# Kernel tuning notes

Hardware: AMD Instinct MI355X
Metric: run time of the kernel (lower is better)

Reference implementation:

```python
import jax, jax.numpy as jnp
import numpy as np
import math

B_CAPS, C_CAPS, K, P, STRIDE, ITERS = 32, 32, 3, 4, 2, 3
PSIZE = P * P
EPS = 1e-8
LAMBDA = 1e-3
LN_2PI = math.log(2.0 * math.pi)


def setup_inputs() -> dict:
    key = jax.random.key(0)
    k1, k2 = jax.random.split(key)
    # input: (b, h, w, B*(P*P+1)); activations must be non-negative (sigmoid-range)
    x = jax.random.uniform(k1, (4, 16, 16, B_CAPS * (PSIZE + 1)), dtype=jnp.float32)
    # nn.Parameter(torch.randn(1, K*K*B, P, P))
    weights = jax.random.normal(k2, (1, K * K * B_CAPS, P, P), dtype=jnp.float32)
    beta_u = jnp.zeros((C_CAPS,), jnp.float32)
    beta_a = jnp.zeros((C_CAPS,), jnp.float32)
    return {"x": x, "weights": weights, "beta_u": beta_u, "beta_a": beta_a}


def _add_patches(x):
    # torch add_pathes: zero-pad 1 on each side, gather KxK patches with stride
    b, h, w, c = x.shape
    x = jnp.pad(x, ((0, 0), (1, 1), (1, 1), (0, 0)))
    hp = h + 2
    oh = (hp - K) // STRIDE + 1
    idxs = np.arange(0, hp - K + 1, STRIDE)[:, None] + np.arange(K)[None, :]  # (oh, K)
    x = x[:, idxs, :, :]        # (b, oh, K, hp, c)
    x = x[:, :, :, idxs, :]     # (b, oh, K, ow, K, c)
    x = jnp.transpose(x, (0, 1, 3, 2, 4, 5))  # (b, oh, ow, K, K, c)
    return x, oh, oh


def _m_step(a_in, r, v, beta_u, beta_a):
    # a_in: (n, Bk, 1), r: (n, Bk, C), v: (n, Bk, C, psize)
    n = v.shape[0]
    r = r * a_in
    r = r / (jnp.sum(r, axis=2, keepdims=True) + EPS)
    r_sum = jnp.sum(r, axis=1, keepdims=True)              # (n, 1, C)
    coeff = (r / (r_sum + EPS))[..., None]                 # (n, Bk, C, 1)
    mu = jnp.sum(coeff * v, axis=1, keepdims=True)         # (n, 1, C, psize)
    sigma_sq = jnp.sum(coeff * (v - mu) ** 2, axis=1, keepdims=True) + EPS
    # cost_h: (n, C, psize)
    cost_h = (beta_u[:, None] + jnp.log(jnp.sqrt(sigma_sq[:, 0]))) * jnp.transpose(r_sum, (0, 2, 1))
    a_out = jax.nn.sigmoid(LAMBDA * (beta_a - jnp.sum(cost_h, axis=2)))  # (n, C)
    return a_out, mu, sigma_sq


def _e_step(mu, sigma_sq, a_out, v):
    ln_p = -(v - mu) ** 2 / (2.0 * sigma_sq) - jnp.log(jnp.sqrt(sigma_sq)) - 0.5 * LN_2PI
    ln_ap = jnp.sum(ln_p, axis=3) + jnp.log(a_out)[:, None, :]  # (n, Bk, C)
    return jax.nn.softmax(ln_ap, axis=2)


def _em_routing(v, a_in, beta_u, beta_a):
    n, Bk, C, _ = v.shape
    r = jnp.full((n, Bk, C), 1.0 / C, dtype=v.dtype)
    mu = a_out = None
    for it in range(ITERS):
        a_out, mu, sigma_sq = _m_step(a_in, r, v, beta_u, beta_a)
        if it < ITERS - 1:
            r = _e_step(mu, sigma_sq, a_out, v)
    return mu, a_out


def reference(x, weights, beta_u, beta_a):
    b = x.shape[0]
    patches, oh, ow = _add_patches(x)                       # (b, oh, ow, K, K, B*(psize+1))
    n = b * oh * ow
    Bk = K * K * B_CAPS
    p_in = patches[..., : B_CAPS * PSIZE].reshape(n, Bk, P, P)
    a_in = patches[..., B_CAPS * PSIZE :].reshape(n, Bk, 1)
    # votes: pose_i @ W_i (weights have no C axis in this repo -> shared across out-caps)
    v = jnp.einsum("nipq,iqr->nipr", p_in, weights[0]).reshape(n, Bk, 1, PSIZE)
    v = jnp.broadcast_to(v, (n, Bk, C_CAPS, PSIZE))
    mu, a_out = _em_routing(v, a_in, beta_u, beta_a)
    p_out = mu.reshape(b, oh, ow, C_CAPS * PSIZE)
    a_out = a_out.reshape(b, oh, ow, C_CAPS)
    return jnp.concatenate([p_out, a_out], axis=-1)        # (b, oh, ow, C*(psize+1))
```

## Files before the change

### kernel.cpp

```cpp
#include <hip/hip_runtime.h>
#include <math.h>

#define NTH 1024

__launch_bounds__(NTH, 4)
__global__ void convcaps_em_kernel(const float* __restrict__ x,
                                   const float* __restrict__ wts,
                                   const float* __restrict__ beta_u,
                                   const float* __restrict__ beta_a,
                                   float* __restrict__ out) {
  constexpr int BK = 288;
  constexpr float EPS = 1e-8f;
  constexpr float LAM = 1e-3f;

  __shared__ __align__(16) float v_lds[BK * 16];
  __shared__ float r_lds[BK * 32];
  __shared__ float w_lds[BK];
  __shared__ float part_lds[32 * 32];
  __shared__ float rsum_lds[32];
  __shared__ __align__(16) float cstat_lds[8 * 32 * 4 * 8];
  __shared__ __align__(8) float muinv_lds[16 * 32 * 2];
  __shared__ float lnac_lds[32];

  const int t = threadIdx.x;
  const int n = blockIdx.x;
  const int b  = n >> 6;
  const int oy = (n >> 3) & 7;
  const int ox = n & 7;

  if (t < BK) {
    const int kk = t >> 5, cap = t & 31;
    const int kh = kk / 3, kw = kk - kh * 3;
    const int iy = oy * 2 - 1 + kh, ix = ox * 2 - 1 + kw;
    float val = 0.0f;
    if ((unsigned)iy < 16u && (unsigned)ix < 16u)
      val = x[(((b * 16 + iy) * 16) + ix) * 544 + 512 + cap];
    w_lds[t] = val / (val + EPS);
  }
  for (int task = t; task < BK * 4; task += NTH) {
    const int i = task >> 2, p = task & 3;
    const int kk = i >> 5, cap = i & 31;
    const int kh = kk / 3, kw = kk - kh * 3;
    const int iy = oy * 2 - 1 + kh, ix = ox * 2 - 1 + kw;
    float4 vv = make_float4(0.f, 0.f, 0.f, 0.f);
    if ((unsigned)iy < 16u && (unsigned)ix < 16u) {
      const float* px = x + ((((b * 16 + iy) * 16) + ix) * 544 + cap * 16 + p * 4);
      const float4 pin = *reinterpret_cast<const float4*>(px);
      const float* pw = wts + i * 16;
      const float4 w0 = *reinterpret_cast<const float4*>(pw + 0);
      const float4 w1 = *reinterpret_cast<const float4*>(pw + 4);
      const float4 w2 = *reinterpret_cast<const float4*>(pw + 8);
      const float4 w3 = *reinterpret_cast<const float4*>(pw + 12);
      vv.x = pin.x * w0.x + pin.y * w1.x + pin.z * w2.x + pin.w * w3.x;
      vv.y = pin.x * w0.y + pin.y * w1.y + pin.z * w2.y + pin.w * w3.y;
      vv.z = pin.x * w0.z + pin.y * w1.z + pin.z * w2.z + pin.w * w3.z;
      vv.w = pin.x * w0.w + pin.y * w1.w + pin.z * w2.w + pin.w * w3.w;
    }
    *reinterpret_cast<float4*>(&v_lds[i * 16 + p * 4]) = vv;
  }
  __syncthreads();

  const int c32 = t & 31;
  const int g32 = t >> 5;

  {
    float colsum = 0.0f;
    #pragma unroll
    for (int pass = 0; pass < 9; ++pass) {
      const int i = pass * 32 + g32;
      const float rv = w_lds[i] * 0.03125f;
      r_lds[i * 32 + c32] = rv;
      colsum += rv;
    }
    part_lds[g32 * 32 + c32] = colsum;
  }
  __syncthreads();

  const int pq = (t >> 5) & 3;
  const int hC = t >> 7;
  const int cS = (t >> 4) & 31;
  const int pS = t & 15;
  const float bu = beta_u[cS];
  const float ba = beta_a[cS];

  for (int it = 0; it < 3; ++it) {
    if (t < 32) {
      float s = 0.0f;
      #pragma unroll
      for (int g = 0; g < 32; ++g) s += part_lds[g * 32 + t];
      rsum_lds[t] = s;
    }
    {
      float4 s1 = make_float4(0.f, 0.f, 0.f, 0.f);
      float4 s2 = make_float4(0.f, 0.f, 0.f, 0.f);
      const int ib = hC * 36;
      #pragma unroll 6
      for (int k = 0; k < 36; ++k) {
        const int i = ib + k;
        const float r = r_lds[i * 32 + c32];
        const float4 v4 = *reinterpret_cast<const float4*>(&v_lds[i * 16 + pq * 4]);
        s1.x = fmaf(r, v4.x, s1.x); s2.x = fmaf(r * v4.x, v4.x, s2.x);
        s1.y = fmaf(r, v4.y, s1.y); s2.y = fmaf(r * v4.y, v4.y, s2.y);
        s1.z = fmaf(r, v4.z, s1.z); s2.z = fmaf(r * v4.z, v4.z, s2.z);
        s1.w = fmaf(r, v4.w, s1.w); s2.w = fmaf(r * v4.w, v4.w, s2.w);
      }
      float* cs = &cstat_lds[(hC * 128 + c32 * 4 + pq) * 8];
      *reinterpret_cast<float4*>(cs + 0) = s1;
      *reinterpret_cast<float4*>(cs + 4) = s2;
    }
    __syncthreads();

    if (t < 512) {
      float s1 = 0.0f, s2 = 0.0f;
      #pragma unroll
      for (int h = 0; h < 8; ++h) {
        const float* cs = &cstat_lds[(h * 128 + cS * 4 + (pS >> 2)) * 8 + (pS & 3)];
        s1 += cs[0];
        s2 += cs[4];
      }
      const float rs = rsum_lds[cS];
      const float D  = rs + EPS;
      const float mu = s1 / D;
      float sig = (s2 - mu * (2.0f * s1 - mu * rs)) / D;
      sig = fmaxf(sig, 0.0f) + EPS;
      const float lhalf = 0.5f * logf(sig);
      float lsum = lhalf;
      #pragma unroll
      for (int m = 8; m >= 1; m >>= 1) lsum += __shfl_xor(lsum, m, 16);
      const float z = LAM * (ba - rs * (16.0f * bu + lsum));
      const float aout = 1.0f / (1.0f + expf(-z));
      if (it < 2) {
        *reinterpret_cast<float2*>(&muinv_lds[(pS * 32 + cS) * 2]) =
            make_float2(mu, 0.5f / sig);
        if (pS == 0) lnac_lds[cS] = logf(aout) - lsum;
      } else {
        out[n * 544 + t] = mu;
        if (pS == 0) out[n * 544 + 512 + cS] = aout;
      }
    }

    if (it < 2) {
      __syncthreads();
      float muc[16], isc[16];
      #pragma unroll
      for (int p2 = 0; p2 < 16; ++p2) {
        const float2 mi =
            *reinterpret_cast<const float2*>(&muinv_lds[(p2 * 32 + c32) * 2]);
        muc[p2] = mi.x;
        isc[p2] = mi.y;
      }
      const float lna = lnac_lds[c32];
      float colsum = 0.0f;
      #pragma unroll 3
      for (int pass = 0; pass < 9; ++pass) {
        const int i = pass * 32 + g32;
        const float4 v0 = *reinterpret_cast<const float4*>(&v_lds[i * 16 + 0]);
        const float4 v1 = *reinterpret_cast<const float4*>(&v_lds[i * 16 + 4]);
        const float4 v2 = *reinterpret_cast<const float4*>(&v_lds[i * 16 + 8]);
        const float4 v3 = *reinterpret_cast<const float4*>(&v_lds[i * 16 + 12]);
        float acc = 0.0f, d;
        d = v0.x - muc[0];  acc = fmaf(d * d, isc[0],  acc);
        d = v0.y - muc[1];  acc = fmaf(d * d, isc[1],  acc);
        d = v0.z - muc[2];  acc = fmaf(d * d, isc[2],  acc);
        d = v0.w - muc[3];  acc = fmaf(d * d, isc[3],  acc);
        d = v1.x - muc[4];  acc = fmaf(d * d, isc[4],  acc);
        d = v1.y - muc[5];  acc = fmaf(d * d, isc[5],  acc);
        d = v1.z - muc[6];  acc = fmaf(d * d, isc[6],  acc);
        d = v1.w - muc[7];  acc = fmaf(d * d, isc[7],  acc);
        d = v2.x - muc[8];  acc = fmaf(d * d, isc[8],  acc);
        d = v2.y - muc[9];  acc = fmaf(d * d, isc[9],  acc);
        d = v2.z - muc[10]; acc = fmaf(d * d, isc[10], acc);
        d = v2.w - muc[11]; acc = fmaf(d * d, isc[11], acc);
        d = v3.x - muc[12]; acc = fmaf(d * d, isc[12], acc);
        d = v3.y - muc[13]; acc = fmaf(d * d, isc[13], acc);
        d = v3.z - muc[14]; acc = fmaf(d * d, isc[14], acc);
        d = v3.w - muc[15]; acc = fmaf(d * d, isc[15], acc);
        const float lnap = lna - acc;
        float mx = lnap;
        #pragma unroll
        for (int m = 16; m >= 1; m >>= 1) mx = fmaxf(mx, __shfl_xor(mx, m, 32));
        const float e = expf(lnap - mx);
        float ss = e;
        #pragma unroll
        for (int m = 16; m >= 1; m >>= 1) ss += __shfl_xor(ss, m, 32);
        const float rn = e * (w_lds[i] / ss);
        r_lds[i * 32 + c32] = rn;
        colsum += rn;
      }
      part_lds[g32 * 32 + c32] = colsum;
      __syncthreads();
    }
  }
}

extern "C" void kernel_launch(void* const* d_in, const int* in_sizes, int n_in,
                              void* d_out, int out_size, void* d_ws, size_t ws_size,
                              hipStream_t stream) {
  const float* x   = (const float*)d_in[0];
  const float* wts = (const float*)d_in[1];
  const float* bu  = (const float*)d_in[2];
  const float* ba  = (const float*)d_in[3];
  float* out = (float*)d_out;
  hipLaunchKernelGGL(convcaps_em_kernel, dim3(256), dim3(NTH), 0, stream,
                     x, wts, bu, ba, out);
}
```

Before: 84.97 us.

## Fuse E-step with M-step accumulation and specialize uniform first M-step

The first M-step is specialized for uniform initial routing: statistics are computed once per pose element and broadcast to all output capsules, instead of running the full per-capsule reduction. Each later E-step now accumulates the weighted first and second moments directly in registers and adds them into shared memory with LDS atomics. This removes the r_lds buffer and the separate M-step pass over v_lds. Fast intrinsics (__expf, __logf) replace expf and logf, trading a little accuracy and adding register pressure and atomic contention.

```diff
diff --git a/kernel.cpp b/kernel.cpp
--- a/kernel.cpp
+++ b/kernel.cpp
@@ -14,13 +14,14 @@
   constexpr float LAM = 1e-3f;
 
   __shared__ __align__(16) float v_lds[BK * 16];
-  __shared__ float r_lds[BK * 32];
   __shared__ float w_lds[BK];
-  __shared__ float part_lds[32 * 32];
+  __shared__ __align__(8) float part_lds[32 * 32];
   __shared__ float rsum_lds[32];
-  __shared__ __align__(16) float cstat_lds[8 * 32 * 4 * 8];
+  __shared__ float s1a_lds[16 * 32];
+  __shared__ float s2a_lds[16 * 32];
   __shared__ __align__(8) float muinv_lds[16 * 32 * 2];
   __shared__ float lnac_lds[32];
+  __shared__ float mu0_lds[16], i2s0_lds[16], sc0_lds[2];
 
   const int t = threadIdx.x;
   const int n = blockIdx.x;
@@ -62,103 +63,82 @@
 
   const int c32 = t & 31;
   const int g32 = t >> 5;
-
-  {
-    float colsum = 0.0f;
-    #pragma unroll
-    for (int pass = 0; pass < 9; ++pass) {
-      const int i = pass * 32 + g32;
-      const float rv = w_lds[i] * 0.03125f;
-      r_lds[i * 32 + c32] = rv;
-      colsum += rv;
-    }
-    part_lds[g32 * 32 + c32] = colsum;
-  }
-  __syncthreads();
-
-  const int pq = (t >> 5) & 3;
-  const int hC = t >> 7;
-  const int cS = (t >> 4) & 31;
-  const int pS = t & 15;
+  const int cS  = (t >> 4) & 31;
+  const int pS  = t & 15;
   const float bu = beta_u[cS];
   const float ba = beta_a[cS];
 
-  for (int it = 0; it < 3; ++it) {
-    if (t < 32) {
-      float s = 0.0f;
-      #pragma unroll
-      for (int g = 0; g < 32; ++g) s += part_lds[g * 32 + t];
-      rsum_lds[t] = s;
-    }
+  if (t < 512) {
+    const int h = t >> 4;
+    float aw = 0.f, a1 = 0.f, a2 = 0.f;
+    #pragma unroll
+    for (int k = 0; k < 9; ++k) {
+      const int i = h * 9 + k;
+      const float wv = w_lds[i];
+      const float vv = v_lds[i * 16 + pS];
+      aw += wv;
+      a1 = fmaf(wv, vv, a1);
+      a2 = fmaf(wv * vv, vv, a2);
+    }
+    *reinterpret_cast<float2*>(&part_lds[(h * 16 + pS) * 2]) = make_float2(a1, a2);
+    if (pS == 0) rsum_lds[h] = aw;
+  }
+  __syncthreads();
+  if (t < 16) {
+    float m0 = 0.f, a1 = 0.f, a2 = 0.f;
+    #pragma unroll
+    for (int h = 0; h < 32; ++h) {
+      m0 += rsum_lds[h];
+      const float2 f2 = *reinterpret_cast<const float2*>(&part_lds[(h * 16 + t) * 2]);
+      a1 += f2.x; a2 += f2.y;
+    }
+    const float D0 = m0 + 32.f * EPS;
+    const float mu = a1 / D0;
+    float sig = (a2 - mu * (2.f * a1 - mu * m0)) / D0;
+    sig = fmaxf(sig, 0.f) + EPS;
+    float ls = 0.5f * __logf(sig);
+    #pragma unroll
+    for (int m = 8; m >= 1; m >>= 1) ls += __shfl_xor(ls, m, 16);
+    mu0_lds[t] = mu;
+    i2s0_lds[t] = 0.5f / sig;
+    if (t == 0) { sc0_lds[0] = m0 * 0.03125f; sc0_lds[1] = ls; }
+  }
+  __syncthreads();
+  if (t < 512) {
+    *reinterpret_cast<float2*>(&muinv_lds[(pS * 32 + cS) * 2]) =
+        make_float2(mu0_lds[pS], i2s0_lds[pS]);
+    s1a_lds[t] = 0.f;
+    s2a_lds[t] = 0.f;
+    if (pS == 0) {
+      const float rs0 = sc0_lds[0], ls = sc0_lds[1];
+      const float z = LAM * (ba - rs0 * (16.f * bu + ls));
+      lnac_lds[cS] = -__logf(1.f + __expf(-z)) - ls;
+    }
+  }
+  __syncthreads();
+
+  for (int it = 0; it < 2; ++it) {
     {
-      float4 s1 = make_float4(0.f, 0.f, 0.f, 0.f);
-      float4 s2 = make_float4(0.f, 0.f, 0.f, 0.f);
-      const int ib = hC * 36;
-      #pragma unroll 6
-      for (int k = 0; k < 36; ++k) {
-        const int i = ib + k;
-        const float r = r_lds[i * 32 + c32];
-        const float4 v4 = *reinterpret_cast<const float4*>(&v_lds[i * 16 + pq * 4]);
-        s1.x = fmaf(r, v4.x, s1.x); s2.x = fmaf(r * v4.x, v4.x, s2.x);
-        s1.y = fmaf(r, v4.y, s1.y); s2.y = fmaf(r * v4.y, v4.y, s2.y);
-        s1.z = fmaf(r, v4.z, s1.z); s2.z = fmaf(r * v4.z, v4.z, s2.z);
-        s1.w = fmaf(r, v4.w, s1.w); s2.w = fmaf(r * v4.w, v4.w, s2.w);
-      }
-      float* cs = &cstat_lds[(hC * 128 + c32 * 4 + pq) * 8];
-      *reinterpret_cast<float4*>(cs + 0) = s1;
-      *reinterpret_cast<float4*>(cs + 4) = s2;
-    }
-    __syncthreads();
-
-    if (t < 512) {
-      float s1 = 0.0f, s2 = 0.0f;
-      #pragma unroll
-      for (int h = 0; h < 8; ++h) {
-        const float* cs = &cstat_lds[(h * 128 + cS * 4 + (pS >> 2)) * 8 + (pS & 3)];
-        s1 += cs[0];
-        s2 += cs[4];
-      }
-      const float rs = rsum_lds[cS];
-      const float D  = rs + EPS;
-      const float mu = s1 / D;
-      float sig = (s2 - mu * (2.0f * s1 - mu * rs)) / D;
-      sig = fmaxf(sig, 0.0f) + EPS;
-      const float lhalf = 0.5f * logf(sig);
-      float lsum = lhalf;
-      #pragma unroll
-      for (int m = 8; m >= 1; m >>= 1) lsum += __shfl_xor(lsum, m, 16);
-      const float z = LAM * (ba - rs * (16.0f * bu + lsum));
-      const float aout = 1.0f / (1.0f + expf(-z));
-      if (it < 2) {
-        *reinterpret_cast<float2*>(&muinv_lds[(pS * 32 + cS) * 2]) =
-            make_float2(mu, 0.5f / sig);
-        if (pS == 0) lnac_lds[cS] = logf(aout) - lsum;
-      } else {
-        out[n * 544 + t] = mu;
-        if (pS == 0) out[n * 544 + 512 + cS] = aout;
-      }
-    }
-
-    if (it < 2) {
-      __syncthreads();
       float muc[16], isc[16];
       #pragma unroll
       for (int p2 = 0; p2 < 16; ++p2) {
         const float2 mi =
             *reinterpret_cast<const float2*>(&muinv_lds[(p2 * 32 + c32) * 2]);
-        muc[p2] = mi.x;
-        isc[p2] = mi.y;
+        muc[p2] = mi.x; isc[p2] = mi.y;
       }
       const float lna = lnac_lds[c32];
-      float colsum = 0.0f;
-      #pragma unroll 3
+      float s1[16], s2[16];
+      #pragma unroll
+      for (int p2 = 0; p2 < 16; ++p2) { s1[p2] = 0.f; s2[p2] = 0.f; }
+      float colsum = 0.f;
+      #pragma unroll 1
       for (int pass = 0; pass < 9; ++pass) {
         const int i = pass * 32 + g32;
         const float4 v0 = *reinterpret_cast<const float4*>(&v_lds[i * 16 + 0]);
         const float4 v1 = *reinterpret_cast<const float4*>(&v_lds[i * 16 + 4]);
         const float4 v2 = *reinterpret_cast<const float4*>(&v_lds[i * 16 + 8]);
         const float4 v3 = *reinterpret_cast<const float4*>(&v_lds[i * 16 + 12]);
-        float acc = 0.0f, d;
+        float acc = 0.f, d;
         d = v0.x - muc[0];  acc = fmaf(d * d, isc[0],  acc);
         d = v0.y - muc[1];  acc = fmaf(d * d, isc[1],  acc);
         d = v0.z - muc[2];  acc = fmaf(d * d, isc[2],  acc);
@@ -179,17 +159,74 @@
         float mx = lnap;
         #pragma unroll
         for (int m = 16; m >= 1; m >>= 1) mx = fmaxf(mx, __shfl_xor(mx, m, 32));
-        const float e = expf(lnap - mx);
+        const float e = __expf(lnap - mx);
         float ss = e;
         #pragma unroll
         for (int m = 16; m >= 1; m >>= 1) ss += __shfl_xor(ss, m, 32);
         const float rn = e * (w_lds[i] / ss);
-        r_lds[i * 32 + c32] = rn;
         colsum += rn;
+        float tv;
+        tv = rn * v0.x; s1[0]  += tv; s2[0]  = fmaf(tv, v0.x, s2[0]);
+        tv = rn * v0.y; s1[1]  += tv; s2[1]  = fmaf(tv, v0.y, s2[1]);
+        tv = rn * v0.z; s1[2]  += tv; s2[2]  = fmaf(tv, v0.z, s2[2]);
+        tv = rn * v0.w; s1[3]  += tv; s2[3]  = fmaf(tv, v0.w, s2[3]);
+        tv = rn * v1.x; s1[4]  += tv; s2[4]  = fmaf(tv, v1.x, s2[4]);
+        tv = rn * v1.y; s1[5]  += tv; s2[5]  = fmaf(tv, v1.y, s2[5]);
+        tv = rn * v1.z; s1[6]  += tv; s2[6]  = fmaf(tv, v1.z, s2[6]);
+        tv = rn * v1.w; s1[7]  += tv; s2[7]  = fmaf(tv, v1.w, s2[7]);
+        tv = rn * v2.x; s1[8]  += tv; s2[8]  = fmaf(tv, v2.x, s2[8]);
+        tv = rn * v2.y; s1[9]  += tv; s2[9]  = fmaf(tv, v2.y, s2[9]);
+        tv = rn * v2.z; s1[10] += tv; s2[10] = fmaf(tv, v2.z, s2[10]);
+        tv = rn * v2.w; s1[11] += tv; s2[11] = fmaf(tv, v2.w, s2[11]);
+        tv = rn * v3.x; s1[12] += tv; s2[12] = fmaf(tv, v3.x, s2[12]);
+        tv = rn * v3.y; s1[13] += tv; s2[13] = fmaf(tv, v3.y, s2[13]);
+        tv = rn * v3.z; s1[14] += tv; s2[14] = fmaf(tv, v3.z, s2[14]);
+        tv = rn * v3.w; s1[15] += tv; s2[15] = fmaf(tv, v3.w, s2[15]);
       }
       part_lds[g32 * 32 + c32] = colsum;
-      __syncthreads();
-    }
+      #pragma unroll
+      for (int p2 = 0; p2 < 16; ++p2) {
+        atomicAdd(&s1a_lds[p2 * 32 + c32], s1[p2]);
+        atomicAdd(&s2a_lds[p2 * 32 + c32], s2[p2]);
+      }
+    }
+    __syncthreads();
+
+    float gs1 = 0.f, gs2 = 0.f;
+    if (t < 512) {
+      gs1 = s1a_lds[pS * 32 + cS];
+      gs2 = s2a_lds[pS * 32 + cS];
+      s1a_lds[pS * 32 + cS] = 0.f;
+      s2a_lds[pS * 32 + cS] = 0.f;
+    } else if (t < 544) {
+      const int c = t - 512;
+      float s = 0.f;
+      #pragma unroll
+      for (int g = 0; g < 32; ++g) s += part_lds[g * 32 + c];
+      rsum_lds[c] = s;
+    }
+    __syncthreads();
+
+    if (t < 512) {
+      const float rs = rsum_lds[cS];
+      const float D = rs + EPS;
+      const float mu = gs1 / D;
+      float sig = (gs2 - mu * (2.f * gs1 - mu * rs)) / D;
+      sig = fmaxf(sig, 0.f) + EPS;
+      float lsum = 0.5f * __logf(sig);
+      #pragma unroll
+      for (int m = 8; m >= 1; m >>= 1) lsum += __shfl_xor(lsum, m, 16);
+      const float z = LAM * (ba - rs * (16.f * bu + lsum));
+      if (it == 0) {
+        *reinterpret_cast<float2*>(&muinv_lds[(pS * 32 + cS) * 2]) =
+            make_float2(mu, 0.5f / sig);
+        if (pS == 0) lnac_lds[cS] = -__logf(1.f + __expf(-z)) - lsum;
+      } else {
+        out[n * 544 + t] = mu;
+        if (pS == 0) out[n * 544 + 512 + cS] = 1.f / (1.f + __expf(-z));
+      }
+    }
+    __syncthreads();
   }
 }
 
```

New measurement: 161.2 us. 1.9x slower.
